# Performance work log

Hardware: AMD Instinct MI355X
Metric: run time of the kernel (lower is better)

The kernel has to match this reference:

```python
import jax, jax.numpy as jnp
import numpy as np

B, T, F = 200, 250, 14
H, D, C = 256, 164, 8


def _lstm(x, W, U, b):
    """Keras-semantics LSTM. x: [B,T,F_in]. Returns (all_h [B,T,H], last_h [B,H]).
    Gate order i, f, c(g), o; sigmoid recurrent activations, tanh cell activation."""
    Bx = x.shape[0]
    units = U.shape[0]
    # precompute input projections for all timesteps: [T, B, 4H]
    xz = jnp.einsum('btf,fk->tbk', x, W) + b

    def step(carry, xz_t):
        h, c = carry
        z = xz_t + h @ U
        i, f, g, o = jnp.split(z, 4, axis=-1)
        i = jax.nn.sigmoid(i)
        f = jax.nn.sigmoid(f)
        g = jnp.tanh(g)
        o = jax.nn.sigmoid(o)
        c = f * c + i * g
        h = o * jnp.tanh(c)
        return (h, c), h

    h0 = jnp.zeros((Bx, units), x.dtype)
    (hT, _), hs = jax.lax.scan(step, (h0, h0), xz)
    return jnp.swapaxes(hs, 0, 1), hT


def setup_inputs() -> dict:
    key = jax.random.key(0)
    ks = jax.random.split(key, 8)
    s = 0.05
    return {
        'inputs': jax.random.normal(ks[0], (B, T, F), jnp.float32),
        'W1': jax.random.normal(ks[1], (F, 4 * H), jnp.float32) * s,
        'U1': jax.random.normal(ks[2], (H, 4 * H), jnp.float32) * s,
        'b1': jnp.zeros((4 * H,), jnp.float32),
        'W2': jax.random.normal(ks[3], (H, 4 * H), jnp.float32) * s,
        'U2': jax.random.normal(ks[4], (H, 4 * H), jnp.float32) * s,
        'b2': jnp.zeros((4 * H,), jnp.float32),
        'Wd': jax.random.normal(ks[5], (H, D), jnp.float32) * s,
        'bd': jnp.zeros((D,), jnp.float32),
        'Ws': jax.random.normal(ks[6], (D, C), jnp.float32) * s,
        'bs': jnp.zeros((C,), jnp.float32),
    }


def reference(inputs, W1, U1, b1, W2, U2, b2, Wd, bd, Ws, bs):
    # LSTM 1: return_sequences=True
    seq, _ = _lstm(inputs, W1, U1, b1)          # [B,T,H]
    # LSTM 2: last hidden state only
    _, h2 = _lstm(seq, W2, U2, b2)              # [B,H]
    hidden = jax.nn.relu(h2 @ Wd + bd)          # [B,D]
    probs = jax.nn.softmax(hidden @ Ws + bs, axis=-1)  # [B,C]
    return probs
```

## Files before the change

### kernel.cpp

```cpp
#include <hip/hip_runtime.h>


#define T_STEPS 250
#define B_REAL  200
#define BPAD    208
#define FIN     14
#define HID     256
#define NGATE   1024
#define NBG     13
#define L1S     2
#define L2S     4
#define SLAB    (BPAD*HID)
#define XT_ROW  32
#define XT_ELEMS (T_STEPS*BPAD*XT_ROW)
#define FSTRIDE 32
#define NF      16
#define F1N     ((long long)T_STEPS*NBG*FSTRIDE)
#define F2N     ((long long)(T_STEPS+1)*NBG*FSTRIDE)

typedef __bf16 bf16_t;
typedef __bf16 bf16x8 __attribute__((ext_vector_type(8)));
typedef float  f32x4  __attribute__((ext_vector_type(4)));

__device__ __forceinline__ float sigmoid_f(float x) {
  return 1.f / (1.f + __expf(-x));
}
__device__ __forceinline__ float tanh_f(float x) {
  float e = __expf(2.f * x);
  return 1.f - 2.f / (e + 1.f);
}

__device__ __forceinline__ unsigned int ld_flag_sc0(const unsigned int* p) {
  unsigned int v;
  asm volatile("global_load_dword %0, %1, off sc0\n\ts_waitcnt vmcnt(0)"
               : "=v"(v) : "v"(p) : "memory");
  return v;
}
__device__ __forceinline__ unsigned int ld_flag_sc01(const unsigned int* p) {
  unsigned int v;
  asm volatile("global_load_dword %0, %1, off sc0 sc1\n\ts_waitcnt vmcnt(0)"
               : "=v"(v) : "v"(p) : "memory");
  return v;
}
__device__ __forceinline__ void st_flag_sc01(unsigned int* p) {
  unsigned int one = 1u;
  asm volatile("global_store_dword %0, %1, off sc0 sc1" :: "v"(p), "v"(one));
}
__device__ __forceinline__ void st_bf16_sc01(bf16_t* p, bf16_t v) {
  unsigned int u = (unsigned int)__builtin_bit_cast(unsigned short, v);
  asm volatile("global_store_short %0, %1, off sc0 sc1" :: "v"(p), "v"(u));
}
__device__ __forceinline__ void waitcnt0() {
  asm volatile("s_waitcnt vmcnt(0)");
}

__device__ __forceinline__ void poll_flags(const unsigned int* rec, int l) {
  int it = 0;
  for (;;) {
    unsigned int v = 1u;
    if (l < NF)
      v = ((it & 7) == 7) ? ld_flag_sc01(rec + l) : ld_flag_sc0(rec + l);
    if (__all(v != 0u)) return;
    ++it;
  }
}

__device__ __forceinline__ long long fidx(int t, int g) {
  return ((long long)t * NBG + g) * FSTRIDE;
}

__global__ void prep_kernel(const float* __restrict__ x,
                            bf16_t* __restrict__ xT,
                            bf16_t* __restrict__ seq,
                            bf16_t* __restrict__ h2seq,
                            unsigned int* __restrict__ f1,
                            unsigned int* __restrict__ f2)
{
  long long i = (long long)blockIdx.x * blockDim.x + threadIdx.x;
  const long long total = (long long)XT_ELEMS + SLAB + SLAB + F1N + F2N;
  if (i >= total) return;
  if (i < XT_ELEMS) {
    int t  = (int)(i / (BPAD * XT_ROW));
    int r  = (int)(i % (BPAD * XT_ROW));
    int b  = r / XT_ROW, kk = r % XT_ROW;
    float v = 0.f;
    if (b < B_REAL && kk < FIN) v = x[((long long)b * T_STEPS + t) * FIN + kk];
    xT[i] = (bf16_t)v;
    return;
  }
  i -= XT_ELEMS;
  if (i < SLAB) { seq[i] = (bf16_t)0.f; return; }
  i -= SLAB;
  if (i < SLAB) { h2seq[i] = (bf16_t)0.f; return; }
  i -= SLAB;
  if (i < F1N) { f1[i] = 0u; return; }
  i -= F1N;
  f2[i] = 0u;
}

__global__ __launch_bounds__(512)
__attribute__((amdgpu_waves_per_eu(2, 2)))
void lstm_fused(
    const float* __restrict__ W1, const float* __restrict__ U1,
    const float* __restrict__ b1,
    const float* __restrict__ W2, const float* __restrict__ U2,
    const float* __restrict__ b2,
    const bf16_t* __restrict__ xT,
    bf16_t* __restrict__ seq, bf16_t* __restrict__ h2s,
    unsigned int* __restrict__ f1, unsigned int* __restrict__ f2)
{
  __shared__ float zs[2][4096];
  const int xcd = blockIdx.x & 7;
  const int slot = blockIdx.x >> 3;
  int g, role;
  if (slot < 6)      { g = xcd;     role = slot; }
  else if (xcd < 5)  { g = 8 + xcd; role = slot - 6; }
  else return;

  const int tid = threadIdx.x;
  const int l   = tid & 63;
  const int lr  = l & 15;
  const int ag  = l >> 4;
  const int w   = tid >> 6;
  const int b0  = g * 16;

  if (role < L1S) {
    const int hsl    = role;
    const int unit   = hsl * 128 + w * 16 + lr;
    const int myslot = hsl * 8 + w;

    f32x4 wb[4][9];
#pragma unroll
    for (int gg = 0; gg < 4; ++gg) {
      const int n = gg * 256 + unit;
#pragma unroll
      for (int kf = 0; kf < 9; ++kf) {
        bf16x8 v;
#pragma unroll
        for (int e = 0; e < 8; ++e) {
          const int k = kf * 32 + ag * 8 + e;
          float val = 0.f;
          if (k < 256)            val = U1[(long long)k * NGATE + n];
          else if (k - 256 < FIN) val = W1[(long long)(k - 256) * NGATE + n];
          v[e] = (bf16_t)val;
        }
        wb[gg][kf] = __builtin_bit_cast(f32x4, v);
      }
    }
    f32x4 bv = { b1[0 * 256 + unit], b1[1 * 256 + unit],
                 b1[2 * 256 + unit], b1[3 * 256 + unit] };
    float cst[4] = {0.f, 0.f, 0.f, 0.f};

    for (int t = 0; t < T_STEPS; ++t) {
#pragma unroll
      for (int gg = 0; gg < 4; ++gg)
#pragma unroll
        for (int kf = 0; kf < 9; ++kf)
          asm volatile("" : "+v"(wb[gg][kf]));
      asm volatile("" : "+v"(bv));

      if (t > 0) poll_flags(f1 + fidx(t - 1, g), l);

      const bf16_t* arow = seq + (long long)t * SLAB + (b0 + lr) * HID;
      f32x4 acc[4] = {{0.f,0.f,0.f,0.f},{0.f,0.f,0.f,0.f},
                      {0.f,0.f,0.f,0.f},{0.f,0.f,0.f,0.f}};
#pragma unroll
      for (int kf = 0; kf < 8; ++kf) {
        const bf16x8 a = *(const bf16x8*)(arow + kf * 32 + ag * 8);
#pragma unroll
        for (int gg = 0; gg < 4; ++gg)
          acc[gg] = __builtin_amdgcn_mfma_f32_16x16x32_bf16(
              a, __builtin_bit_cast(bf16x8, wb[gg][kf]), acc[gg], 0, 0, 0);
      }
      {
        const bf16x8 ax = *(const bf16x8*)(xT + ((long long)t * BPAD + b0 + lr) * XT_ROW + ag * 8);
#pragma unroll
        for (int gg = 0; gg < 4; ++gg)
          acc[gg] = __builtin_amdgcn_mfma_f32_16x16x32_bf16(
              ax, __builtin_bit_cast(bf16x8, wb[gg][8]), acc[gg], 0, 0, 0);
      }
      bf16_t* orow = seq + (long long)(t + 1) * SLAB;
#pragma unroll
      for (int r = 0; r < 4; ++r) {
        const float ig = sigmoid_f(acc[0][r] + bv[0]);
        const float fg = sigmoid_f(acc[1][r] + bv[1]);
        const float gg = tanh_f  (acc[2][r] + bv[2]);
        const float og = sigmoid_f(acc[3][r] + bv[3]);
        const float c  = fg * cst[r] + ig * gg;
        cst[r] = c;
        st_bf16_sc01(orow + (b0 + ag * 4 + r) * HID + unit,
                     (bf16_t)(og * tanh_f(c)));
      }
      waitcnt0();
      if (l == 0) st_flag_sc01(f1 + fidx(t, g) + myslot);
    }
  } else {
    const int hsl    = role - L1S;
    const int uq     = w & 3;
    const int kh     = w >> 2;
    const int unit   = hsl * 64 + uq * 16 + lr;
    const int myslot = hsl * 4 + uq;

    const float* Wsrc = kh ? W2 : U2;
    f32x4 wb[4][8];
#pragma unroll
    for (int gg = 0; gg < 4; ++gg) {
      const int n = gg * 256 + unit;
#pragma unroll
      for (int kf = 0; kf < 8; ++kf) {
        bf16x8 v;
#pragma unroll
        for (int e = 0; e < 8; ++e)
          v[e] = (bf16_t)Wsrc[(long long)(kf * 32 + ag * 8 + e) * NGATE + n];
        wb[gg][kf] = __builtin_bit_cast(f32x4, v);
      }
    }
    f32x4 bv = { b2[0 * 256 + unit], b2[1 * 256 + unit],
                 b2[2 * 256 + unit], b2[3 * 256 + unit] };
    float cst[4] = {0.f, 0.f, 0.f, 0.f};

    for (int t = 0; t < T_STEPS; ++t) {
#pragma unroll
      for (int gg = 0; gg < 4; ++gg)
#pragma unroll
        for (int kf = 0; kf < 8; ++kf)
          asm volatile("" : "+v"(wb[gg][kf]));
      asm volatile("" : "+v"(bv));

      if (kh == 1)      poll_flags(f1 + fidx(t, g), l);
      else if (t > 0)   poll_flags(f2 + fidx(t, g), l);

      const bf16_t* arow = kh
          ? (seq + (long long)(t + 1) * SLAB + (b0 + lr) * HID)
          : (h2s + (long long)t       * SLAB + (b0 + lr) * HID);
      f32x4 acc[4] = {{0.f,0.f,0.f,0.f},{0.f,0.f,0.f,0.f},
                      {0.f,0.f,0.f,0.f},{0.f,0.f,0.f,0.f}};
#pragma unroll
      for (int kf = 0; kf < 8; ++kf) {
        const bf16x8 a = *(const bf16x8*)(arow + kf * 32 + ag * 8);
#pragma unroll
        for (int gg = 0; gg < 4; ++gg)
          acc[gg] = __builtin_amdgcn_mfma_f32_16x16x32_bf16(
              a, __builtin_bit_cast(bf16x8, wb[gg][kf]), acc[gg], 0, 0, 0);
      }
      if (kh == 1) {
        float* z = zs[t & 1];
#pragma unroll
        for (int gg = 0; gg < 4; ++gg)
#pragma unroll
          for (int r = 0; r < 4; ++r)
            z[((gg * 4 + uq) * 16 + ag * 4 + r) * 16 + lr] = acc[gg][r];
      }
      __syncthreads();
      if (kh == 0) {
        const float* z = zs[t & 1];
        bf16_t* orow = h2s + (long long)(t + 1) * SLAB;
#pragma unroll
        for (int r = 0; r < 4; ++r) {
          const int row = ag * 4 + r;
          const float zi = acc[0][r] + z[((0 * 4 + uq) * 16 + row) * 16 + lr] + bv[0];
          const float zf = acc[1][r] + z[((1 * 4 + uq) * 16 + row) * 16 + lr] + bv[1];
          const float zg = acc[2][r] + z[((2 * 4 + uq) * 16 + row) * 16 + lr] + bv[2];
          const float zo = acc[3][r] + z[((3 * 4 + uq) * 16 + row) * 16 + lr] + bv[3];
          const float ig = sigmoid_f(zi);
          const float fg = sigmoid_f(zf);
          const float gg = tanh_f(zg);
          const float og = sigmoid_f(zo);
          const float c  = fg * cst[r] + ig * gg;
          cst[r] = c;
          st_bf16_sc01(orow + (b0 + row) * HID + unit,
                       (bf16_t)(og * tanh_f(c)));
        }
        waitcnt0();
        if (l == 0) st_flag_sc01(f2 + fidx(t + 1, g) + myslot);
      }
    }
  }
}

__global__ __launch_bounds__(64) void head_kernel(
    const bf16_t* __restrict__ h2,
    const float* __restrict__ Wd, const float* __restrict__ bd,
    const float* __restrict__ Ws, const float* __restrict__ bs,
    float* __restrict__ out)
{
  __shared__ float hsm[HID];
  __shared__ float hid[164];
  __shared__ float lg[8];
  const int b = blockIdx.x, tid = threadIdx.x;
  const bf16_t* hr = h2 + (long long)b * HID;
  for (int k = tid; k < HID; k += 64) hsm[k] = (float)hr[k];
  __syncthreads();
  for (int d = tid; d < 164; d += 64) {
    float a = bd[d];
    for (int k = 0; k < HID; ++k) a = fmaf(hsm[k], Wd[k * 164 + d], a);
    hid[d] = fmaxf(a, 0.f);
  }
  __syncthreads();
  if (tid < 8) {
    float a = bs[tid];
    for (int k = 0; k < 164; ++k) a = fmaf(hid[k], Ws[k * 8 + tid], a);
    lg[tid] = a;
  }
  __syncthreads();
  if (tid < 8) {
    float m = lg[0];
#pragma unroll
    for (int j = 1; j < 8; ++j) m = fmaxf(m, lg[j]);
    float s = 0.f;
#pragma unroll
    for (int j = 0; j < 8; ++j) s += __expf(lg[j] - m);
    out[b * 8 + tid] = __expf(lg[tid] - m) / s;
  }
}

extern "C" void kernel_launch(void* const* d_in, const int* in_sizes, int n_in,
                              void* d_out, int out_size, void* d_ws, size_t ws_size,
                              hipStream_t stream)
{
  const float* x  = (const float*)d_in[0];
  const float* W1 = (const float*)d_in[1];
  const float* U1 = (const float*)d_in[2];
  const float* b1 = (const float*)d_in[3];
  const float* W2 = (const float*)d_in[4];
  const float* U2 = (const float*)d_in[5];
  const float* b2 = (const float*)d_in[6];
  const float* Wd = (const float*)d_in[7];
  const float* bd = (const float*)d_in[8];
  const float* Ws = (const float*)d_in[9];
  const float* bs = (const float*)d_in[10];
  (void)in_sizes; (void)n_in; (void)out_size; (void)ws_size;

  char* p = (char*)d_ws;
  size_t off = 0;
  auto carve = [&](size_t bytes) -> void* {
    void* r = p + off;
    off = (off + bytes + 255) & ~(size_t)255;
    return r;
  };
  bf16_t* xT  = (bf16_t*)carve((size_t)XT_ELEMS * 2);
  bf16_t* seq = (bf16_t*)carve((size_t)(T_STEPS + 1) * SLAB * 2);
  bf16_t* h2s = (bf16_t*)carve((size_t)(T_STEPS + 1) * SLAB * 2);
  unsigned int* f1 = (unsigned int*)carve((size_t)F1N * 4);
  unsigned int* f2 = (unsigned int*)carve((size_t)F2N * 4);

  const long long prep_total = (long long)XT_ELEMS + SLAB + SLAB + F1N + F2N;
  const int pb = (int)((prep_total + 255) / 256);

  prep_kernel<<<pb, 256, 0, stream>>>(x, xT, seq, h2s, f1, f2);
  lstm_fused<<<96, 512, 0, stream>>>(W1, U1, b1, W2, U2, b2,
                                     xT, seq, h2s, f1, f2);
  head_kernel<<<B_REAL, 64, 0, stream>>>(h2s + (long long)T_STEPS * SLAB,
                                         Wd, bd, Ws, bs, (float*)d_out);
}
```

Before: 1.328 ms.

## Publish hidden state with sc0 stores first, defer system-scope writes and flag reposting

Each recurrent step now writes h with plain stores and raises its flag with an sc0 store, then re-stores h with sc0 sc1 afterwards. Pollers use only sc0 loads for the first 64 iterations. After that they re-post their own flag at system scope and switch to periodic sc0 sc1 loads, which covers producers whose data sits in another cache domain. The bias is folded into the MFMA accumulator init and weights are pinned to AGPRs. The goal is a shorter per-step handoff between cooperating blocks, at the cost of relying on subtle cross-XCD coherence behaviour and a timeout-based fallback.

```diff
diff --git a/kernel.cpp b/kernel.cpp
--- a/kernel.cpp
+++ b/kernel.cpp
@@ -42,26 +42,41 @@
                : "=v"(v) : "v"(p) : "memory");
   return v;
 }
+__device__ __forceinline__ void st_flag_sc0(unsigned int* p) {
+  unsigned int one = 1u;
+  asm volatile("global_store_dword %0, %1, off sc0" :: "v"(p), "v"(one) : "memory");
+}
 __device__ __forceinline__ void st_flag_sc01(unsigned int* p) {
   unsigned int one = 1u;
-  asm volatile("global_store_dword %0, %1, off sc0 sc1" :: "v"(p), "v"(one));
+  asm volatile("global_store_dword %0, %1, off sc0 sc1" :: "v"(p), "v"(one) : "memory");
 }
 __device__ __forceinline__ void st_bf16_sc01(bf16_t* p, bf16_t v) {
   unsigned int u = (unsigned int)__builtin_bit_cast(unsigned short, v);
-  asm volatile("global_store_short %0, %1, off sc0 sc1" :: "v"(p), "v"(u));
+  asm volatile("global_store_short %0, %1, off sc0 sc1" :: "v"(p), "v"(u) : "memory");
 }
 __device__ __forceinline__ void waitcnt0() {
-  asm volatile("s_waitcnt vmcnt(0)");
-}
-
-__device__ __forceinline__ void poll_flags(const unsigned int* rec, int l) {
+  asm volatile("s_waitcnt vmcnt(0)" ::: "memory");
+}
+
+template <bool CAN_POST>
+__device__ __forceinline__ void poll_flags(const unsigned int* rec, int l,
+                                           int myslot) {
   int it = 0;
   for (;;) {
     unsigned int v = 1u;
-    if (l < NF)
-      v = ((it & 7) == 7) ? ld_flag_sc01(rec + l) : ld_flag_sc0(rec + l);
+    if (l < NF) v = ld_flag_sc0(rec + l);
     if (__all(v != 0u)) return;
     ++it;
+    if (it == 64) {
+      waitcnt0();
+      if (CAN_POST && l == 0)
+        st_flag_sc01(const_cast<unsigned int*>(rec) + myslot);
+    }
+    if (it > 64 && (it & 7) == 0) {
+      v = 1u;
+      if (l < NF) v = ld_flag_sc01(rec + l);
+      if (__all(v != 0u)) return;
+    }
   }
 }
 
@@ -147,8 +162,9 @@
         wb[gg][kf] = __builtin_bit_cast(f32x4, v);
       }
     }
-    f32x4 bv = { b1[0 * 256 + unit], b1[1 * 256 + unit],
-                 b1[2 * 256 + unit], b1[3 * 256 + unit] };
+    float bias[4];
+#pragma unroll
+    for (int gg = 0; gg < 4; ++gg) bias[gg] = b1[gg * 256 + unit];
     float cst[4] = {0.f, 0.f, 0.f, 0.f};
 
     for (int t = 0; t < T_STEPS; ++t) {
@@ -156,14 +172,15 @@
       for (int gg = 0; gg < 4; ++gg)
 #pragma unroll
         for (int kf = 0; kf < 9; ++kf)
-          asm volatile("" : "+v"(wb[gg][kf]));
-      asm volatile("" : "+v"(bv));
-
-      if (t > 0) poll_flags(f1 + fidx(t - 1, g), l);
+          asm volatile("" : "+a"(wb[gg][kf]));
+
+      if (t > 0) poll_flags<true>(f1 + fidx(t - 1, g), l, myslot);
 
       const bf16_t* arow = seq + (long long)t * SLAB + (b0 + lr) * HID;
-      f32x4 acc[4] = {{0.f,0.f,0.f,0.f},{0.f,0.f,0.f,0.f},
-                      {0.f,0.f,0.f,0.f},{0.f,0.f,0.f,0.f}};
+      f32x4 acc[4];
+#pragma unroll
+      for (int gg = 0; gg < 4; ++gg)
+        acc[gg] = (f32x4){bias[gg], bias[gg], bias[gg], bias[gg]};
 #pragma unroll
       for (int kf = 0; kf < 8; ++kf) {
         const bf16x8 a = *(const bf16x8*)(arow + kf * 32 + ag * 8);
@@ -180,20 +197,26 @@
               ax, __builtin_bit_cast(bf16x8, wb[gg][8]), acc[gg], 0, 0, 0);
       }
       bf16_t* orow = seq + (long long)(t + 1) * SLAB;
+      bf16_t hv[4];
 #pragma unroll
       for (int r = 0; r < 4; ++r) {
-        const float ig = sigmoid_f(acc[0][r] + bv[0]);
-        const float fg = sigmoid_f(acc[1][r] + bv[1]);
-        const float gg = tanh_f  (acc[2][r] + bv[2]);
-        const float og = sigmoid_f(acc[3][r] + bv[3]);
+        const float ig = sigmoid_f(acc[0][r]);
+        const float fg = sigmoid_f(acc[1][r]);
+        const float gg = tanh_f  (acc[2][r]);
+        const float og = sigmoid_f(acc[3][r]);
         const float c  = fg * cst[r] + ig * gg;
         cst[r] = c;
-        st_bf16_sc01(orow + (b0 + ag * 4 + r) * HID + unit,
-                     (bf16_t)(og * tanh_f(c)));
+        hv[r] = (bf16_t)(og * tanh_f(c));
+        orow[(b0 + ag * 4 + r) * HID + unit] = hv[r];
       }
       waitcnt0();
-      if (l == 0) st_flag_sc01(f1 + fidx(t, g) + myslot);
-    }
+      if (l == 0) st_flag_sc0(f1 + fidx(t, g) + myslot);
+#pragma unroll
+      for (int r = 0; r < 4; ++r)
+        st_bf16_sc01(orow + (b0 + ag * 4 + r) * HID + unit, hv[r]);
+    }
+    waitcnt0();
+    if (l == 0) st_flag_sc01(f1 + fidx(T_STEPS - 1, g) + myslot);
   } else {
     const int hsl    = role - L1S;
     const int uq     = w & 3;
@@ -215,8 +238,9 @@
         wb[gg][kf] = __builtin_bit_cast(f32x4, v);
       }
     }
-    f32x4 bv = { b2[0 * 256 + unit], b2[1 * 256 + unit],
-                 b2[2 * 256 + unit], b2[3 * 256 + unit] };
+    float bias[4];
+#pragma unroll
+    for (int gg = 0; gg < 4; ++gg) bias[gg] = b2[gg * 256 + unit];
     float cst[4] = {0.f, 0.f, 0.f, 0.f};
 
     for (int t = 0; t < T_STEPS; ++t) {
@@ -224,17 +248,19 @@
       for (int gg = 0; gg < 4; ++gg)
 #pragma unroll
         for (int kf = 0; kf < 8; ++kf)
-          asm volatile("" : "+v"(wb[gg][kf]));
-      asm volatile("" : "+v"(bv));
-
-      if (kh == 1)      poll_flags(f1 + fidx(t, g), l);
-      else if (t > 0)   poll_flags(f2 + fidx(t, g), l);
+          asm volatile("" : "+a"(wb[gg][kf]));
+
+      if (kh == 1)      poll_flags<false>(f1 + fidx(t, g), l, 0);
+      else if (t > 0)   poll_flags<true>(f2 + fidx(t, g), l, myslot);
 
       const bf16_t* arow = kh
           ? (seq + (long long)(t + 1) * SLAB + (b0 + lr) * HID)
           : (h2s + (long long)t       * SLAB + (b0 + lr) * HID);
-      f32x4 acc[4] = {{0.f,0.f,0.f,0.f},{0.f,0.f,0.f,0.f},
-                      {0.f,0.f,0.f,0.f},{0.f,0.f,0.f,0.f}};
+      f32x4 acc[4];
+#pragma unroll
+      for (int gg = 0; gg < 4; ++gg)
+        acc[gg] = kh ? (f32x4){0.f, 0.f, 0.f, 0.f}
+                     : (f32x4){bias[gg], bias[gg], bias[gg], bias[gg]};
 #pragma unroll
       for (int kf = 0; kf < 8; ++kf) {
         const bf16x8 a = *(const bf16x8*)(arow + kf * 32 + ag * 8);
@@ -255,24 +281,28 @@
       if (kh == 0) {
         const float* z = zs[t & 1];
         bf16_t* orow = h2s + (long long)(t + 1) * SLAB;
+        bf16_t hv[4];
 #pragma unroll
         for (int r = 0; r < 4; ++r) {
           const int row = ag * 4 + r;
-          const float zi = acc[0][r] + z[((0 * 4 + uq) * 16 + row) * 16 + lr] + bv[0];
-          const float zf = acc[1][r] + z[((1 * 4 + uq) * 16 + row) * 16 + lr] + bv[1];
-          const float zg = acc[2][r] + z[((2 * 4 + uq) * 16 + row) * 16 + lr] + bv[2];
-          const float zo = acc[3][r] + z[((3 * 4 + uq) * 16 + row) * 16 + lr] + bv[3];
+          const float zi = acc[0][r] + z[((0 * 4 + uq) * 16 + row) * 16 + lr];
+          const float zf = acc[1][r] + z[((1 * 4 + uq) * 16 + row) * 16 + lr];
+          const float zg = acc[2][r] + z[((2 * 4 + uq) * 16 + row) * 16 + lr];
+          const float zo = acc[3][r] + z[((3 * 4 + uq) * 16 + row) * 16 + lr];
           const float ig = sigmoid_f(zi);
           const float fg = sigmoid_f(zf);
           const float gg = tanh_f(zg);
           const float og = sigmoid_f(zo);
           const float c  = fg * cst[r] + ig * gg;
           cst[r] = c;
-          st_bf16_sc01(orow + (b0 + row) * HID + unit,
-                       (bf16_t)(og * tanh_f(c)));
+          hv[r] = (bf16_t)(og * tanh_f(c));
+          orow[(b0 + row) * HID + unit] = hv[r];
         }
         waitcnt0();
-        if (l == 0) st_flag_sc01(f2 + fidx(t + 1, g) + myslot);
+        if (l == 0) st_flag_sc0(f2 + fidx(t + 1, g) + myslot);
+#pragma unroll
+        for (int r = 0; r < 4; ++r)
+          st_bf16_sc01(orow + (b0 + ag * 4 + r) * HID + unit, hv[r]);
       }
     }
   }
```

Result: slower. 2.491 ms (+87.6%).
